# Kernel optimization log

Hardware: AMD Instinct MI355X
Metric: run time of the kernel (lower is better)

## Reference

```python
import jax, jax.numpy as jnp
import numpy as np
import math

D_MODEL = 1024
NUM_HEADS = 16
D_HEAD = D_MODEL // NUM_HEADS


def setup_inputs() -> dict:
    key = jax.random.key(0)
    k1, k2, k3, k4, k5 = jax.random.split(key, 5)
    scale = 1.0 / math.sqrt(D_MODEL)
    x = jax.random.normal(k1, (4, 2048, D_MODEL), dtype=jnp.float32)
    W_qkv = jax.random.normal(k2, (D_MODEL, 3 * D_MODEL), dtype=jnp.float32) * scale
    b_qkv = jax.random.normal(k3, (3 * D_MODEL,), dtype=jnp.float32) * 0.02
    W_o = jax.random.normal(k4, (D_MODEL, D_MODEL), dtype=jnp.float32) * scale
    b_o = jax.random.normal(k5, (D_MODEL,), dtype=jnp.float32) * 0.02
    return {"x": x, "W_qkv": W_qkv, "b_qkv": b_qkv, "W_o": W_o, "b_o": b_o}


def reference(x, W_qkv, b_qkv, W_o, b_o):
    B, C, D = x.shape
    H, Dh = NUM_HEADS, D_HEAD
    qkv = x @ W_qkv + b_qkv                       # [B, C, 3D]
    qkv = qkv.reshape(B, C, 3, H, Dh).transpose(2, 0, 3, 1, 4)  # [3, B, H, C, Dh]
    Q, K, V = qkv[0], qkv[1], qkv[2]
    scores = jnp.einsum('bhqd,bhkd->bhqk', Q, K) / math.sqrt(Dh)  # [B, H, C, C]
    causal = jnp.tril(jnp.ones((C, C), dtype=bool))
    scores = jnp.where(causal, scores, -jnp.inf)
    weights = jax.nn.softmax(scores, axis=-1)
    attn = jnp.einsum('bhqk,bhkd->bhqd', weights, V)              # [B, H, C, Dh]
    attn = attn.transpose(0, 2, 1, 3).reshape(B, C, D)
    return attn @ W_o + b_o
```

## Files before the change

### kernel.cpp

```cpp
#include <hip/hip_runtime.h>
#include <hip/hip_bf16.h>
#include <stdint.h>


typedef __attribute__((ext_vector_type(8))) short short8;
typedef __attribute__((ext_vector_type(4))) short short4v;
typedef __attribute__((ext_vector_type(4))) float f32x4;

#define AS1 __attribute__((address_space(1)))
#define AS3 __attribute__((address_space(3)))

static __device__ __forceinline__ short f2bf(float f) {
  union { float f; uint32_t u; } v; v.f = f;
  uint32_t r = v.u + 0x7fffu + ((v.u >> 16) & 1u);
  return (short)(r >> 16);
}

static __device__ __forceinline__ short f2bfh(float f) {
  __hip_bfloat16 h = __float2bfloat16(f);
  return *reinterpret_cast<short*>(&h);
}

static __device__ __forceinline__ void gload_lds16(const void* g, void* l) {
  __builtin_amdgcn_global_load_lds((const AS1 void*)g, (AS3 void*)l, 16, 0, 0);
}

#define MFMA16(a, b, c) __builtin_amdgcn_mfma_f32_16x16x32_bf16((a), (b), (c), 0, 0, 0)

__global__ __launch_bounds__(256) void k_cvt_x(const float* __restrict__ x,
                                               short* __restrict__ xb) {
  long i = ((long)blockIdx.x * 256 + threadIdx.x) * 4;
  const float4 v = *(const float4*)(x + i);
  short4v o;
  o[0] = f2bf(v.x); o[1] = f2bf(v.y); o[2] = f2bf(v.z); o[3] = f2bf(v.w);
  *(short4v*)(xb + i) = o;
}

__global__ __launch_bounds__(256) void k_transpose_bf(const float* __restrict__ W,
                                                      short* __restrict__ Wt,
                                                      int K, int N) {
  __shared__ float t[64][65];
  const int nb = blockIdx.x * 64, kb = blockIdx.y * 64;
  const int tid = threadIdx.x;
#pragma unroll
  for (int i = 0; i < 16; ++i) {
    int idx = i * 256 + tid; int r = idx >> 6, c = idx & 63;
    t[r][c] = W[(long)(kb + r) * N + nb + c];
  }
  __syncthreads();
#pragma unroll
  for (int i = 0; i < 16; ++i) {
    int idx = i * 256 + tid; int r = idx >> 6, c = idx & 63;
    Wt[(long)(nb + r) * K + kb + c] = f2bf(t[c][r]);
  }
}

template <int EPI>
__global__ __launch_bounds__(256)
void k_gemm(const short* __restrict__ A, const short* __restrict__ Bt,
            const float* __restrict__ bias, float* __restrict__ Cf,
            short* __restrict__ q_ws, short* __restrict__ k_ws, short* __restrict__ vt_ws,
            int M, int N, int K) {
  __shared__ __align__(16) short a_sh[2][128 * 32];
  __shared__ __align__(16) short b_sh[2][128 * 32];
  const int tid = threadIdx.x;
  const int lane = tid & 63, wid = tid >> 6;
  const int l15 = lane & 15, lg = lane >> 4;
  const int wr = wid >> 1, wc = wid & 1;
  const int m0 = blockIdx.y * 128, n0 = blockIdx.x * 128;

  f32x4 acc[4][4] = {};

  const int r0 = tid >> 2, g0 = tid & 3;
  const short* ga0 = A + (long)(m0 + r0) * K + g0 * 8;
  const short* gb0 = Bt + (long)(n0 + r0) * K + g0 * 8;

#define GSTAGE(buf, ks)                                                             \
  {                                                                                 \
    _Pragma("unroll")                                                               \
    for (int i = 0; i < 2; ++i) {                                                   \
      gload_lds16(ga0 + (long)i * 64 * K + (ks), &a_sh[buf][(i * 256 + tid) * 8]);  \
      gload_lds16(gb0 + (long)i * 64 * K + (ks), &b_sh[buf][(i * 256 + tid) * 8]);  \
    }                                                                               \
  }

  GSTAGE(0, 0);
  __syncthreads();

  const int nt = K >> 5;
  int cur = 0;
  for (int t = 0; t < nt; ++t) {
    if (t + 1 < nt) GSTAGE(cur ^ 1, (t + 1) * 32);

    short8 af[4], bfr[4];
#pragma unroll
    for (int m = 0; m < 4; ++m)
      af[m] = *(const short8*)(&a_sh[cur][(wr * 64 + m * 16 + l15) * 32 + lg * 8]);
#pragma unroll
    for (int n = 0; n < 4; ++n)
      bfr[n] = *(const short8*)(&b_sh[cur][(wc * 64 + n * 16 + l15) * 32 + lg * 8]);
#pragma unroll
    for (int m = 0; m < 4; ++m)
#pragma unroll
      for (int n = 0; n < 4; ++n)
        acc[m][n] = MFMA16(af[m], bfr[n], acc[m][n]);

    __syncthreads();
    cur ^= 1;
  }
#undef GSTAGE

#pragma unroll
  for (int mm = 0; mm < 4; ++mm) {
#pragma unroll
    for (int nn = 0; nn < 4; ++nn) {
      const int n = n0 + wc * 64 + nn * 16 + l15;
      const int mb = m0 + wr * 64 + mm * 16 + lg * 4;
      if (EPI == 1) {
#pragma unroll
        for (int r = 0; r < 4; ++r)
          Cf[(long)(mb + r) * N + n] = acc[mm][nn][r] + bias[n];
      } else {
        const int which = n >> 10;
        const int h = (n >> 6) & 15, d = n & 63;
        const int b = mb >> 11, c = mb & 2047;
        const int bh = b * 16 + h;
        const float bi = bias[n];
        if (which == 2) {
          short4v o;
#pragma unroll
          for (int r = 0; r < 4; ++r) o[r] = f2bf(acc[mm][nn][r] + bi);
          *(short4v*)(vt_ws + ((long)bh * 64 + d) * 2048 + c) = o;
        } else if (which == 0) {
#pragma unroll
          for (int r = 0; r < 4; ++r)
            q_ws[((long)bh * 2048 + c + r) * 64 + d] = f2bf((acc[mm][nn][r] + bi) * 0.18033688011f);
        } else {
#pragma unroll
          for (int r = 0; r < 4; ++r)
            k_ws[((long)bh * 2048 + c + r) * 64 + d] = f2bf(acc[mm][nn][r] + bi);
        }
      }
    }
  }
}

__global__ __launch_bounds__(128)
void k_attn(const short* __restrict__ q_ws, const short* __restrict__ k_ws,
            const short* __restrict__ vt_ws, short* __restrict__ attn_out) {
  __shared__ __align__(16) short k_sh[2][64 * 64];
  __shared__ __align__(16) short v_sh[2][64 * 64];

  const int tid = threadIdx.x;
  const int lane = tid & 63, wid = tid >> 6;
  const int l15 = lane & 15, lg = lane >> 4;
  const int bh = blockIdx.x;
  const int qt = (int)gridDim.y - 1 - (int)blockIdx.y;
  const int b = bh >> 4, h = bh & 15;
  const int qwA = qt * 64 + wid * 16;
  const int qwB = qwA + 32;
  const int qA = qwA + l15, qB = qwB + l15;
  const int nt = qt + 1;

  const short* qrowA = q_ws + ((long)bh * 2048 + qA) * 64;
  const short* qrowB = q_ws + ((long)bh * 2048 + qB) * 64;
  const short8 qfA0 = *(const short8*)(qrowA + lg * 8);
  const short8 qfA1 = *(const short8*)(qrowA + 32 + lg * 8);
  const short8 qfB0 = *(const short8*)(qrowB + lg * 8);
  const short8 qfB1 = *(const short8*)(qrowB + 32 + lg * 8);

  const int s7 = l15 & 7;
  const int koff0 = ((lg ^ s7) << 4);
  const int koff1 = (((4 + lg) ^ s7) << 4);
  const int vsub = (lg & 1) * 8, vg = lg >> 1;
  int voff[4];
#pragma unroll
  for (int m2 = 0; m2 < 4; ++m2)
    voff[m2] = (((2 * m2 + vg) ^ s7) << 4) | vsub;

  f32x4 accA[4] = {}, accB[4] = {};
  float lA = 0.f, lB = 0.f;

  const int srow = tid >> 3, sg = tid & 7;

#define STAGE(buf, kv)                                                              \
  {                                                                                 \
    _Pragma("unroll")                                                               \
    for (int i = 0; i < 4; ++i) {                                                   \
      int row = i * 16 + srow;                                                      \
      int gl = sg ^ (row & 7);                                                      \
      gload_lds16(k_ws + ((long)bh * 2048 + (kv) + row) * 64 + gl * 8,              \
                  &k_sh[buf][(i * 128 + tid) * 8]);                                 \
      gload_lds16(vt_ws + ((long)bh * 64 + row) * 2048 + (kv) + gl * 8,             \
                  &v_sh[buf][(i * 128 + tid) * 8]);                                 \
    }                                                                               \
  }

  STAGE(0, 0);
  asm volatile("s_waitcnt vmcnt(0)" ::: "memory");
  __syncthreads();

  int cur = 0;
  for (int t = 0; t < nt; ++t) {
    const int kv0 = t * 64;
    if (t + 1 < nt) STAGE(cur ^ 1, kv0 + 64);

    const char* ksh = (const char*)k_sh[cur];
    const char* vsh = (const char*)v_sh[cur];

    f32x4 stA[4], stB[4];
    __builtin_amdgcn_s_setprio(1);
#pragma unroll
    for (int j = 0; j < 4; ++j) {
      const char* kr = ksh + (j * 16 + l15) * 128;
      short8 kf0 = *(const short8*)(kr + koff0);
      short8 kf1 = *(const short8*)(kr + koff1);
      f32x4 zA = {};
      zA = MFMA16(kf0, qfA0, zA);
      zA = MFMA16(kf1, qfA1, zA);
      stA[j] = zA;
      f32x4 zB = {};
      zB = MFMA16(kf0, qfB0, zB);
      zB = MFMA16(kf1, qfB1, zB);
      stB[j] = zB;
    }
    __builtin_amdgcn_s_setprio(0);

    if (t == nt - 1) {
#pragma unroll
      for (int j = 0; j < 4; ++j) {
        int kvr = kv0 + j * 16 + lg * 4;
#pragma unroll
        for (int r = 0; r < 4; ++r) {
          if (kvr + r > qA) stA[j][r] = -1e30f;
          if (kvr + r > qB) stB[j][r] = -1e30f;
        }
      }
    }

    short8 pA0, pA1, pB0, pB1;
    {
      float ps = 0.f;
#pragma unroll
      for (int j = 0; j < 4; ++j)
#pragma unroll
        for (int r = 0; r < 4; ++r) {
          float e = __builtin_amdgcn_exp2f(stA[j][r]);
          stA[j][r] = e;
          ps += e;
        }
      lA += ps;
#pragma unroll
      for (int r = 0; r < 4; ++r) {
        pA0[r]     = f2bfh(stA[0][r]);
        pA0[4 + r] = f2bfh(stA[1][r]);
        pA1[r]     = f2bfh(stA[2][r]);
        pA1[4 + r] = f2bfh(stA[3][r]);
      }
    }
    {
      float ps = 0.f;
#pragma unroll
      for (int j = 0; j < 4; ++j)
#pragma unroll
        for (int r = 0; r < 4; ++r) {
          float e = __builtin_amdgcn_exp2f(stB[j][r]);
          stB[j][r] = e;
          ps += e;
        }
      lB += ps;
#pragma unroll
      for (int r = 0; r < 4; ++r) {
        pB0[r]     = f2bfh(stB[0][r]);
        pB0[4 + r] = f2bfh(stB[1][r]);
        pB1[r]     = f2bfh(stB[2][r]);
        pB1[4 + r] = f2bfh(stB[3][r]);
      }
    }

    __builtin_amdgcn_s_setprio(1);
#pragma unroll
    for (int dt = 0; dt < 4; ++dt) {
      const char* vr = vsh + (dt * 16 + l15) * 128;
      union { short8 s8; short4v s4[2]; } vf1, vf2;
      vf1.s4[0] = *(const short4v*)(vr + voff[0]);
      vf1.s4[1] = *(const short4v*)(vr + voff[1]);
      vf2.s4[0] = *(const short4v*)(vr + voff[2]);
      vf2.s4[1] = *(const short4v*)(vr + voff[3]);
      accA[dt] = MFMA16(vf1.s8, pA0, accA[dt]);
      accA[dt] = MFMA16(vf2.s8, pA1, accA[dt]);
      accB[dt] = MFMA16(vf1.s8, pB0, accB[dt]);
      accB[dt] = MFMA16(vf2.s8, pB1, accB[dt]);
    }
    __builtin_amdgcn_s_setprio(0);

    asm volatile("s_waitcnt vmcnt(0)" ::: "memory");
    __syncthreads();
    cur ^= 1;
  }
#undef STAGE

  {
    float lt = lA;
    lt += __shfl_xor(lt, 16);
    lt += __shfl_xor(lt, 32);
    const float inv = 1.0f / lt;
    short* obase = attn_out + ((long)b * 2048 + qA) * 1024 + h * 64;
#pragma unroll
    for (int dt = 0; dt < 4; ++dt) {
      short4v o;
#pragma unroll
      for (int r = 0; r < 4; ++r) o[r] = f2bfh(accA[dt][r] * inv);
      *(short4v*)(obase + dt * 16 + lg * 4) = o;
    }
  }
  {
    float lt = lB;
    lt += __shfl_xor(lt, 16);
    lt += __shfl_xor(lt, 32);
    const float inv = 1.0f / lt;
    short* obase = attn_out + ((long)b * 2048 + qB) * 1024 + h * 64;
#pragma unroll
    for (int dt = 0; dt < 4; ++dt) {
      short4v o;
#pragma unroll
      for (int r = 0; r < 4; ++r) o[r] = f2bfh(accB[dt][r] * inv);
      *(short4v*)(obase + dt * 16 + lg * 4) = o;
    }
  }
}

extern "C" void kernel_launch(void* const* d_in, const int* in_sizes, int n_in,
                              void* d_out, int out_size, void* d_ws, size_t ws_size,
                              hipStream_t stream) {
  const float* x     = (const float*)d_in[0];
  const float* W_qkv = (const float*)d_in[1];
  const float* b_qkv = (const float*)d_in[2];
  const float* W_o   = (const float*)d_in[3];
  const float* b_o   = (const float*)d_in[4];
  float* out = (float*)d_out;

  char* ws = (char*)d_ws;
  short* x_bf   = (short*)(ws);
  short* wqkv_t = (short*)(ws + 16777216);
  short* wo_t   = (short*)(ws + 23068672);
  short* q_ws   = (short*)(ws + 25165824);
  short* k_ws   = (short*)(ws + 41943040);
  short* vt_ws  = (short*)(ws + 58720256);

  k_cvt_x<<<dim3(8192), dim3(256), 0, stream>>>(x, x_bf);
  k_transpose_bf<<<dim3(48, 16), dim3(256), 0, stream>>>(W_qkv, wqkv_t, 1024, 3072);
  k_transpose_bf<<<dim3(16, 16), dim3(256), 0, stream>>>(W_o, wo_t, 1024, 1024);
  k_gemm<0><<<dim3(24, 64), dim3(256), 0, stream>>>(x_bf, wqkv_t, b_qkv, nullptr,
                                                    q_ws, k_ws, vt_ws, 8192, 3072, 1024);
  k_attn<<<dim3(64, 32), dim3(128), 0, stream>>>(q_ws, k_ws, vt_ws, x_bf);
  k_gemm<1><<<dim3(8, 64), dim3(256), 0, stream>>>(x_bf, wo_t, b_o, out,
                                                   nullptr, nullptr, nullptr, 8192, 1024, 1024);
}
```

Before: 171.5 us.

## Restructure GEMM into 128x256 tiles with swizzled LDS and split-phase pipelining

The GEMM kernel now uses 512-thread blocks computing 128x256 tiles with a K-step of 64. LDS rows are XOR-swizzled to avoid bank conflicts, and each iteration is split into two halves that interleave async global-to-LDS prefetch with MFMA work, using explicit vmcnt waits, s_barrier and setprio. This targets load latency, LDS conflicts and barrier overhead in the QKV and output projections. It adds larger LDS use (96KB per block), fewer blocks (768 and 256), and fragile hand-tuned wait counts.

```diff
diff --git a/kernel.cpp b/kernel.cpp
--- a/kernel.cpp
+++ b/kernel.cpp
@@ -56,89 +56,141 @@
 }
 
 template <int EPI>
-__global__ __launch_bounds__(256)
+__global__ __launch_bounds__(512, 2)
 void k_gemm(const short* __restrict__ A, const short* __restrict__ Bt,
             const float* __restrict__ bias, float* __restrict__ Cf,
             short* __restrict__ q_ws, short* __restrict__ k_ws, short* __restrict__ vt_ws,
             int M, int N, int K) {
-  __shared__ __align__(16) short a_sh[2][128 * 32];
-  __shared__ __align__(16) short b_sh[2][128 * 32];
+  __shared__ __align__(16) short a_sh[2][128 * 64];
+  __shared__ __align__(16) short b_sh[2][256 * 64];
   const int tid = threadIdx.x;
   const int lane = tid & 63, wid = tid >> 6;
   const int l15 = lane & 15, lg = lane >> 4;
-  const int wr = wid >> 1, wc = wid & 1;
-  const int m0 = blockIdx.y * 128, n0 = blockIdx.x * 128;
-
-  f32x4 acc[4][4] = {};
-
-  const int r0 = tid >> 2, g0 = tid & 3;
-  const short* ga0 = A + (long)(m0 + r0) * K + g0 * 8;
-  const short* gb0 = Bt + (long)(n0 + r0) * K + g0 * 8;
-
-#define GSTAGE(buf, ks)                                                             \
-  {                                                                                 \
-    _Pragma("unroll")                                                               \
-    for (int i = 0; i < 2; ++i) {                                                   \
-      gload_lds16(ga0 + (long)i * 64 * K + (ks), &a_sh[buf][(i * 256 + tid) * 8]);  \
-      gload_lds16(gb0 + (long)i * 64 * K + (ks), &b_sh[buf][(i * 256 + tid) * 8]);  \
-    }                                                                               \
-  }
-
-  GSTAGE(0, 0);
-  __syncthreads();
-
-  const int nt = K >> 5;
+  const int s7 = l15 & 7;
+  const int wgm = wid >> 2, wgn = wid & 3;
+  const int m0 = blockIdx.y * 128, n0 = blockIdx.x * 256;
+
+  f32x4 acc[2][4][2] = {};
+
+  const int srow = tid >> 3, sgr = tid & 7;
+
+#define STAGE_A(buf, kb, j)                                                          \
+  {                                                                                  \
+    int row = (j) * 64 + srow;                                                       \
+    gload_lds16(A + (long)(m0 + row) * K + (kb) + ((sgr ^ (row & 7)) << 3),          \
+                &a_sh[buf][((j) * 512 + tid) * 8]);                                  \
+  }
+#define STAGE_B(buf, kb, j)                                                          \
+  {                                                                                  \
+    int row = (j) * 64 + srow;                                                       \
+    gload_lds16(Bt + (long)(n0 + row) * K + (kb) + ((sgr ^ (row & 7)) << 3),         \
+                &b_sh[buf][((j) * 512 + tid) * 8]);                                  \
+  }
+
+  STAGE_A(0, 0, 0); STAGE_A(0, 0, 1);
+  STAGE_B(0, 0, 0); STAGE_B(0, 0, 1); STAGE_B(0, 0, 2); STAGE_B(0, 0, 3);
+  asm volatile("s_waitcnt vmcnt(2)" ::: "memory");
+  __builtin_amdgcn_sched_barrier(0);
+  __builtin_amdgcn_s_barrier();
+
+  const int nt = K >> 6;
   int cur = 0;
   for (int t = 0; t < nt; ++t) {
-    if (t + 1 < nt) GSTAGE(cur ^ 1, (t + 1) * 32);
-
-    short8 af[4], bfr[4];
-#pragma unroll
-    for (int m = 0; m < 4; ++m)
-      af[m] = *(const short8*)(&a_sh[cur][(wr * 64 + m * 16 + l15) * 32 + lg * 8]);
-#pragma unroll
-    for (int n = 0; n < 4; ++n)
-      bfr[n] = *(const short8*)(&b_sh[cur][(wc * 64 + n * 16 + l15) * 32 + lg * 8]);
-#pragma unroll
-    for (int m = 0; m < 4; ++m)
-#pragma unroll
-      for (int n = 0; n < 4; ++n)
-        acc[m][n] = MFMA16(af[m], bfr[n], acc[m][n]);
-
-    __syncthreads();
+    const int kb2 = (t + 1) << 6;
+    const bool pre = (t + 1 < nt);
+
+    short8 af[4][2], bf[2][2];
+#pragma unroll
+    for (int mi = 0; mi < 4; ++mi)
+#pragma unroll
+      for (int kk = 0; kk < 2; ++kk) {
+        const int row = (wgm * 4 + mi) * 16 + l15;
+        af[mi][kk] = *(const short8*)(&a_sh[cur][row * 64 + (((kk * 4 + lg) ^ s7) << 3)]);
+      }
+#pragma unroll
+    for (int ni = 0; ni < 2; ++ni)
+#pragma unroll
+      for (int kk = 0; kk < 2; ++kk) {
+        const int row = (wgn * 2 + ni) * 16 + l15;
+        bf[ni][kk] = *(const short8*)(&b_sh[cur][row * 64 + (((kk * 4 + lg) ^ s7) << 3)]);
+      }
+    if (pre) { STAGE_A(cur ^ 1, kb2, 0); STAGE_A(cur ^ 1, kb2, 1); STAGE_B(cur ^ 1, kb2, 0); }
+    __builtin_amdgcn_s_barrier();
+    __builtin_amdgcn_s_setprio(1);
+#pragma unroll
+    for (int mi = 0; mi < 4; ++mi)
+#pragma unroll
+      for (int ni = 0; ni < 2; ++ni)
+#pragma unroll
+        for (int kk = 0; kk < 2; ++kk)
+          acc[0][mi][ni] = MFMA16(af[mi][kk], bf[ni][kk], acc[0][mi][ni]);
+    __builtin_amdgcn_s_setprio(0);
+    if (pre) asm volatile("s_waitcnt vmcnt(3)" ::: "memory");
+    else     asm volatile("s_waitcnt vmcnt(0)" ::: "memory");
+    __builtin_amdgcn_sched_barrier(0);
+    __builtin_amdgcn_s_barrier();
+
+    short8 bg[2][2];
+#pragma unroll
+    for (int ni = 0; ni < 2; ++ni)
+#pragma unroll
+      for (int kk = 0; kk < 2; ++kk) {
+        const int row = 128 + (wgn * 2 + ni) * 16 + l15;
+        bg[ni][kk] = *(const short8*)(&b_sh[cur][row * 64 + (((kk * 4 + lg) ^ s7) << 3)]);
+      }
+    if (pre) { STAGE_B(cur ^ 1, kb2, 1); STAGE_B(cur ^ 1, kb2, 2); STAGE_B(cur ^ 1, kb2, 3); }
+    __builtin_amdgcn_s_barrier();
+    __builtin_amdgcn_s_setprio(1);
+#pragma unroll
+    for (int mi = 0; mi < 4; ++mi)
+#pragma unroll
+      for (int ni = 0; ni < 2; ++ni)
+#pragma unroll
+        for (int kk = 0; kk < 2; ++kk)
+          acc[1][mi][ni] = MFMA16(af[mi][kk], bg[ni][kk], acc[1][mi][ni]);
+    __builtin_amdgcn_s_setprio(0);
+    if (pre) {
+      asm volatile("s_waitcnt vmcnt(2)" ::: "memory");
+      __builtin_amdgcn_sched_barrier(0);
+    }
+    __builtin_amdgcn_s_barrier();
     cur ^= 1;
   }
-#undef GSTAGE
-
-#pragma unroll
-  for (int mm = 0; mm < 4; ++mm) {
-#pragma unroll
-    for (int nn = 0; nn < 4; ++nn) {
-      const int n = n0 + wc * 64 + nn * 16 + l15;
-      const int mb = m0 + wr * 64 + mm * 16 + lg * 4;
-      if (EPI == 1) {
-#pragma unroll
-        for (int r = 0; r < 4; ++r)
-          Cf[(long)(mb + r) * N + n] = acc[mm][nn][r] + bias[n];
-      } else {
-        const int which = n >> 10;
-        const int h = (n >> 6) & 15, d = n & 63;
-        const int b = mb >> 11, c = mb & 2047;
-        const int bh = b * 16 + h;
-        const float bi = bias[n];
-        if (which == 2) {
-          short4v o;
-#pragma unroll
-          for (int r = 0; r < 4; ++r) o[r] = f2bf(acc[mm][nn][r] + bi);
-          *(short4v*)(vt_ws + ((long)bh * 64 + d) * 2048 + c) = o;
-        } else if (which == 0) {
+#undef STAGE_A
+#undef STAGE_B
+
+#pragma unroll
+  for (int h = 0; h < 2; ++h) {
+#pragma unroll
+    for (int mi = 0; mi < 4; ++mi) {
+#pragma unroll
+      for (int ni = 0; ni < 2; ++ni) {
+        const int n = n0 + h * 128 + (wgn * 2 + ni) * 16 + l15;
+        const int mb = m0 + (wgm * 4 + mi) * 16 + lg * 4;
+        if (EPI == 1) {
 #pragma unroll
           for (int r = 0; r < 4; ++r)
-            q_ws[((long)bh * 2048 + c + r) * 64 + d] = f2bf((acc[mm][nn][r] + bi) * 0.18033688011f);
+            Cf[(long)(mb + r) * N + n] = acc[h][mi][ni][r] + bias[n];
         } else {
-#pragma unroll
-          for (int r = 0; r < 4; ++r)
-            k_ws[((long)bh * 2048 + c + r) * 64 + d] = f2bf(acc[mm][nn][r] + bi);
+          const int which = n >> 10;
+          const int hh = (n >> 6) & 15, d = n & 63;
+          const int b = mb >> 11, c = mb & 2047;
+          const int bh = b * 16 + hh;
+          const float bi = bias[n];
+          if (which == 2) {
+            short4v o;
+#pragma unroll
+            for (int r = 0; r < 4; ++r) o[r] = f2bf(acc[h][mi][ni][r] + bi);
+            *(short4v*)(vt_ws + ((long)bh * 64 + d) * 2048 + c) = o;
+          } else if (which == 0) {
+#pragma unroll
+            for (int r = 0; r < 4; ++r)
+              q_ws[((long)bh * 2048 + c + r) * 64 + d] = f2bf((acc[h][mi][ni][r] + bi) * 0.18033688011f);
+          } else {
+#pragma unroll
+            for (int r = 0; r < 4; ++r)
+              k_ws[((long)bh * 2048 + c + r) * 64 + d] = f2bf(acc[h][mi][ni][r] + bi);
+          }
         }
       }
     }
@@ -351,9 +403,9 @@
   k_cvt_x<<<dim3(8192), dim3(256), 0, stream>>>(x, x_bf);
   k_transpose_bf<<<dim3(48, 16), dim3(256), 0, stream>>>(W_qkv, wqkv_t, 1024, 3072);
   k_transpose_bf<<<dim3(16, 16), dim3(256), 0, stream>>>(W_o, wo_t, 1024, 1024);
-  k_gemm<0><<<dim3(24, 64), dim3(256), 0, stream>>>(x_bf, wqkv_t, b_qkv, nullptr,
+  k_gemm<0><<<dim3(12, 64), dim3(512), 0, stream>>>(x_bf, wqkv_t, b_qkv, nullptr,
                                                     q_ws, k_ws, vt_ws, 8192, 3072, 1024);
   k_attn<<<dim3(64, 32), dim3(128), 0, stream>>>(q_ws, k_ws, vt_ws, x_bf);
-  k_gemm<1><<<dim3(8, 64), dim3(256), 0, stream>>>(x_bf, wo_t, b_o, out,
+  k_gemm<1><<<dim3(4, 64), dim3(512), 0, stream>>>(x_bf, wo_t, b_o, out,
                                                    nullptr, nullptr, nullptr, 8192, 1024, 1024);
 }
```

Result: no change. 170.9 us (-0.4%).

## Enlarge GEMM tiles to 256x256 with 8 waves and 4-stage LDS pipeline

Applied to the files above, without the earlier changes.

Reworks the bf16 MFMA GEMM to use 256x256 block tiles computed by 512 threads (8 waves, each owning 128x64). Global-to-LDS loads now run through a 4-buffer ring with prefetch depth 3, using explicit vmcnt waits and raw s_barrier in place of a double buffer with __syncthreads. Wave priority is raised around the MFMA block. The goal is more data reuse per LDS load and better hiding of memory latency. The cost is 128KB of LDS per block, which limits occupancy, and much smaller grids (384 and 128 blocks), which may leave CUs idle on the output projection.

```diff
diff --git a/kernel.cpp b/kernel.cpp
--- a/kernel.cpp
+++ b/kernel.cpp
@@ -56,89 +56,104 @@
 }
 
 template <int EPI>
-__global__ __launch_bounds__(256)
+__global__ __launch_bounds__(512, 2)
 void k_gemm(const short* __restrict__ A, const short* __restrict__ Bt,
             const float* __restrict__ bias, float* __restrict__ Cf,
             short* __restrict__ q_ws, short* __restrict__ k_ws, short* __restrict__ vt_ws,
             int M, int N, int K) {
-  __shared__ __align__(16) short a_sh[2][128 * 32];
-  __shared__ __align__(16) short b_sh[2][128 * 32];
+  __shared__ __align__(16) short a_sh[4][256 * 32];
+  __shared__ __align__(16) short b_sh[4][256 * 32];
   const int tid = threadIdx.x;
   const int lane = tid & 63, wid = tid >> 6;
   const int l15 = lane & 15, lg = lane >> 4;
-  const int wr = wid >> 1, wc = wid & 1;
-  const int m0 = blockIdx.y * 128, n0 = blockIdx.x * 128;
-
-  f32x4 acc[4][4] = {};
-
-  const int r0 = tid >> 2, g0 = tid & 3;
-  const short* ga0 = A + (long)(m0 + r0) * K + g0 * 8;
-  const short* gb0 = Bt + (long)(n0 + r0) * K + g0 * 8;
-
-#define GSTAGE(buf, ks)                                                             \
-  {                                                                                 \
-    _Pragma("unroll")                                                               \
-    for (int i = 0; i < 2; ++i) {                                                   \
-      gload_lds16(ga0 + (long)i * 64 * K + (ks), &a_sh[buf][(i * 256 + tid) * 8]);  \
-      gload_lds16(gb0 + (long)i * 64 * K + (ks), &b_sh[buf][(i * 256 + tid) * 8]);  \
-    }                                                                               \
-  }
-
-  GSTAGE(0, 0);
-  __syncthreads();
+  const int wgm = wid >> 2, wgn = wid & 3;
+  const int m0 = blockIdx.y * 256, n0 = blockIdx.x * 256;
+
+  f32x4 acc[8][4] = {};
+
+  const int srow = tid >> 2, sg = tid & 3;
+  const short* ga0 = A + (long)(m0 + srow) * K + sg * 8;
+  const short* gb0 = Bt + (long)(n0 + srow) * K + sg * 8;
+
+#define STAGE_A2(buf, ks)                                                      \
+  {                                                                            \
+    gload_lds16(ga0 + (ks), &a_sh[buf][tid * 8]);                              \
+    gload_lds16(ga0 + (long)128 * K + (ks), &a_sh[buf][4096 + tid * 8]);       \
+  }
+#define STAGE_B2(buf, ks)                                                      \
+  {                                                                            \
+    gload_lds16(gb0 + (ks), &b_sh[buf][tid * 8]);                              \
+    gload_lds16(gb0 + (long)128 * K + (ks), &b_sh[buf][4096 + tid * 8]);       \
+  }
+#define STAGE4(buf, ks) { STAGE_A2(buf, ks); STAGE_B2(buf, ks); }
+
+  STAGE4(0, 0); STAGE4(1, 32); STAGE4(2, 64);
+  asm volatile("s_waitcnt vmcnt(8)" ::: "memory");
+  __builtin_amdgcn_sched_barrier(0);
+  __builtin_amdgcn_s_barrier();
 
   const int nt = K >> 5;
-  int cur = 0;
   for (int t = 0; t < nt; ++t) {
-    if (t + 1 < nt) GSTAGE(cur ^ 1, (t + 1) * 32);
-
-    short8 af[4], bfr[4];
-#pragma unroll
-    for (int m = 0; m < 4; ++m)
-      af[m] = *(const short8*)(&a_sh[cur][(wr * 64 + m * 16 + l15) * 32 + lg * 8]);
-#pragma unroll
-    for (int n = 0; n < 4; ++n)
-      bfr[n] = *(const short8*)(&b_sh[cur][(wc * 64 + n * 16 + l15) * 32 + lg * 8]);
-#pragma unroll
-    for (int m = 0; m < 4; ++m)
-#pragma unroll
-      for (int n = 0; n < 4; ++n)
-        acc[m][n] = MFMA16(af[m], bfr[n], acc[m][n]);
-
-    __syncthreads();
-    cur ^= 1;
-  }
-#undef GSTAGE
-
-#pragma unroll
-  for (int mm = 0; mm < 4; ++mm) {
-#pragma unroll
-    for (int nn = 0; nn < 4; ++nn) {
-      const int n = n0 + wc * 64 + nn * 16 + l15;
-      const int mb = m0 + wr * 64 + mm * 16 + lg * 4;
+    const int rd = t & 3, wr = (t + 3) & 3;
+    const int ks3 = (t + 3) << 5;
+
+    short8 af[8], bfr[4];
+#pragma unroll
+    for (int mi = 0; mi < 8; ++mi)
+      af[mi] = *(const short8*)(&a_sh[rd][(wgm * 128 + mi * 16 + l15) * 32 + lg * 8]);
+    if (t + 3 < nt) STAGE_A2(wr, ks3);
+#pragma unroll
+    for (int ni = 0; ni < 4; ++ni)
+      bfr[ni] = *(const short8*)(&b_sh[rd][(wgn * 64 + ni * 16 + l15) * 32 + lg * 8]);
+    if (t + 3 < nt) STAGE_B2(wr, ks3);
+
+    __builtin_amdgcn_s_setprio(1);
+#pragma unroll
+    for (int mi = 0; mi < 8; ++mi)
+#pragma unroll
+      for (int ni = 0; ni < 4; ++ni)
+        acc[mi][ni] = MFMA16(af[mi], bfr[ni], acc[mi][ni]);
+    __builtin_amdgcn_s_setprio(0);
+
+    if (t + 3 < nt)      asm volatile("s_waitcnt vmcnt(8)" ::: "memory");
+    else if (t + 2 < nt) asm volatile("s_waitcnt vmcnt(4)" ::: "memory");
+    else                 asm volatile("s_waitcnt vmcnt(0)" ::: "memory");
+    __builtin_amdgcn_sched_barrier(0);
+    __builtin_amdgcn_s_barrier();
+  }
+#undef STAGE_A2
+#undef STAGE_B2
+#undef STAGE4
+
+#pragma unroll
+  for (int mi = 0; mi < 8; ++mi) {
+#pragma unroll
+    for (int ni = 0; ni < 4; ++ni) {
+      const int n = n0 + wgn * 64 + ni * 16 + l15;
+      const int mb = m0 + wgm * 128 + mi * 16 + lg * 4;
       if (EPI == 1) {
 #pragma unroll
         for (int r = 0; r < 4; ++r)
-          Cf[(long)(mb + r) * N + n] = acc[mm][nn][r] + bias[n];
+          Cf[(long)(mb + r) * N + n] = acc[mi][ni][r] + bias[n];
       } else {
         const int which = n >> 10;
-        const int h = (n >> 6) & 15, d = n & 63;
+        const int hh = (n >> 6) & 15, d = n & 63;
         const int b = mb >> 11, c = mb & 2047;
-        const int bh = b * 16 + h;
+        const int bh = b * 16 + hh;
         const float bi = bias[n];
         if (which == 2) {
           short4v o;
 #pragma unroll
-          for (int r = 0; r < 4; ++r) o[r] = f2bf(acc[mm][nn][r] + bi);
+          for (int r = 0; r < 4; ++r) o[r] = f2bf(acc[mi][ni][r] + bi);
           *(short4v*)(vt_ws + ((long)bh * 64 + d) * 2048 + c) = o;
         } else if (which == 0) {
 #pragma unroll
           for (int r = 0; r < 4; ++r)
-            q_ws[((long)bh * 2048 + c + r) * 64 + d] = f2bf((acc[mm][nn][r] + bi) * 0.18033688011f);
+            q_ws[((long)bh * 2048 + c + r) * 64 + d] = f2bf((acc[mi][ni][r] + bi) * 0.18033688011f);
         } else {
 #pragma unroll
           for (int r = 0; r < 4; ++r)
-            k_ws[((long)bh * 2048 + c + r) * 64 + d] = f2bf(acc[mm][nn][r] + bi);
+            k_ws[((long)bh * 2048 + c + r) * 64 + d] = f2bf(acc[mi][ni][r] + bi);
         }
       }
     }
@@ -351,9 +366,9 @@
   k_cvt_x<<<dim3(8192), dim3(256), 0, stream>>>(x, x_bf);
   k_transpose_bf<<<dim3(48, 16), dim3(256), 0, stream>>>(W_qkv, wqkv_t, 1024, 3072);
   k_transpose_bf<<<dim3(16, 16), dim3(256), 0, stream>>>(W_o, wo_t, 1024, 1024);
-  k_gemm<0><<<dim3(24, 64), dim3(256), 0, stream>>>(x_bf, wqkv_t, b_qkv, nullptr,
+  k_gemm<0><<<dim3(12, 32), dim3(512), 0, stream>>>(x_bf, wqkv_t, b_qkv, nullptr,
                                                     q_ws, k_ws, vt_ws, 8192, 3072, 1024);
   k_attn<<<dim3(64, 32), dim3(128), 0, stream>>>(q_ws, k_ws, vt_ws, x_bf);
-  k_gemm<1><<<dim3(8, 64), dim3(256), 0, stream>>>(x_bf, wo_t, b_o, out,
+  k_gemm<1><<<dim3(4, 32), dim3(512), 0, stream>>>(x_bf, wo_t, b_o, out,
                                                    nullptr, nullptr, nullptr, 8192, 1024, 1024);
 }
```

Result: slower. 179.5 us (+4.7%).
